# Kernel optimization log

Measured on AMD Instinct MI355X. Metric: run time of the kernel, lower is better.

Reference implementation:

```python
import jax, jax.numpy as jnp
import numpy as np

N_FEATURES = 4096
N_ACTIONS = 4
N_CLAUSES_PER_ACTION = 10
N_CLAUSES = N_ACTIONS * N_CLAUSES_PER_ACTION
BATCH = 16384
EPS = 1e-8
ACTIVE_THRESH = 1e-6


def setup_inputs() -> dict:
    key = jax.random.key(0)
    k1, k2, k3, k4 = jax.random.split(key, 4)
    features = jax.random.uniform(k1, (BATCH, N_FEATURES), dtype=jnp.float32)
    # nn.Parameter(torch.randn(F, C) * 2.0)
    clause_weights = jax.random.normal(k2, (N_FEATURES, N_CLAUSES), dtype=jnp.float32) * 2.0
    # nn.Parameter(torch.randn(F, C) * 0.5 + 2.0)
    mask_logits = jax.random.normal(k3, (N_FEATURES, N_CLAUSES), dtype=jnp.float32) * 0.5 + 2.0
    # gumbel/concrete uniform noise (torch.rand_like(mask_logits)), fixed for determinism
    u = jax.random.uniform(k4, (N_FEATURES, N_CLAUSES), dtype=jnp.float32)
    temperature = jnp.float32(5.0)
    return {"features": features, "clause_weights": clause_weights,
            "mask_logits": mask_logits, "u": u, "temperature": temperature}


def reference(features, clause_weights, mask_logits, u, temperature):
    # --- sample_mask (training: concrete relaxation) ---
    s = jax.nn.sigmoid((jnp.log(u + EPS) - jnp.log(1.0 - u + EPS) + mask_logits)
                       / (temperature + EPS))                     # (F, C)
    # --- get_clause_weights (training: soft ternary * mask) ---
    w = jnp.tanh(clause_weights / (temperature + EPS)) * s        # (F, C)

    # --- evaluate all clauses at once (masked literal mean) ---
    # literal = where(w > 0, x, 1 - x), restricted to active features (|w| > 1e-6).
    # sum_f active*literal = x @ A_pos + (1 - x) @ A_neg, so no (B,F,C) intermediate.
    active = jnp.abs(w) > ACTIVE_THRESH
    pos = (active & (w > 0)).astype(features.dtype)               # (F, C)
    neg = (active & ~(w > 0)).astype(features.dtype)              # (F, C)
    num = features @ pos + (1.0 - features) @ neg                 # (B, C)
    cnt = pos.sum(axis=0) + neg.sum(axis=0)                       # (C,)
    # mean over active literals; empty clause -> satisfaction 1
    sat = jnp.where(cnt > 0, num / jnp.maximum(cnt, 1.0), 1.0)    # (B, C)

    # --- per-action segment sum (assignment = arange(C) // cpa, contiguous) ---
    B = features.shape[0]
    action_scores = sat.reshape(B, N_ACTIONS, N_CLAUSES_PER_ACTION).sum(axis=-1)
    return action_scores                                          # (B, n_actions)
```

## Files before the change

### kernel.cpp

```cpp
#include <hip/hip_runtime.h>
#include <hip/hip_bf16.h>

#define N_FEATURES 4096
#define N_ACTIONS 4
#define N_CPA 10
#define N_CLAUSES 40
#define BATCH 16384
#define EPS 1e-8f
#define ACTIVE_THRESH 1e-6f
#define NBLK_A 160

typedef float f4v __attribute__((ext_vector_type(4)));

__global__ void count_kernel(const float* __restrict__ cw,
                             const float* __restrict__ ml,
                             const float* __restrict__ u,
                             const float* __restrict__ tptr,
                             signed char* __restrict__ d8,
                             float* __restrict__ part_pos,
                             float* __restrict__ part_neg)
{
    __shared__ float sp[N_CLAUSES], sn[N_CLAUSES];
    const int tid = threadIdx.x;
    if (tid < N_CLAUSES) { sp[tid] = 0.0f; sn[tid] = 0.0f; }
    __syncthreads();

    const float invt = 1.0f / (tptr[0] + EPS);
    const int i4 = blockIdx.x * 256 + tid;

    const float4 u4 = ((const float4*)u)[i4];
    const float4 m4 = ((const float4*)ml)[i4];
    const float4 c4 = ((const float4*)cw)[i4];

    const float uu[4] = {u4.x, u4.y, u4.z, u4.w};
    const float mm[4] = {m4.x, m4.y, m4.z, m4.w};
    const float ww[4] = {c4.x, c4.y, c4.z, c4.w};

    union { signed char c[4]; int i; } pk;
    #pragma unroll
    for (int e = 0; e < 4; ++e) {
        float z = (__logf((uu[e] + EPS) / (1.0f - uu[e] + EPS)) + mm[e]) * invt;
        float s = 1.0f / (1.0f + __expf(-z));
        float w = tanhf(ww[e] * invt) * s;
        bool active = fabsf(w) > ACTIVE_THRESH;
        bool pos = active && (w > 0.0f);
        bool neg = active && !(w > 0.0f);
        pk.c[e] = pos ? 1 : (neg ? -1 : 0);
        const int c = (i4 * 4 + e) % N_CLAUSES;
        if (pos) atomicAdd(&sp[c], 1.0f);
        if (neg) atomicAdd(&sn[c], 1.0f);
    }
    ((int*)d8)[i4] = pk.i;

    __syncthreads();
    if (tid < N_CLAUSES) {
        part_pos[blockIdx.x * N_CLAUSES + tid] = sp[tid];
        part_neg[blockIdx.x * N_CLAUSES + tid] = sn[tid];
    }
}

__global__ void fold_kernel(const signed char* __restrict__ d8,
                            const float* __restrict__ part_pos,
                            const float* __restrict__ part_neg,
                            float* __restrict__ D,
                            float* __restrict__ K)
{
    __shared__ float sinv[N_CLAUSES], sneg[N_CLAUSES];
    const int tid = threadIdx.x;
    if (tid < N_CLAUSES) {
        float p = 0.0f, n = 0.0f;
        for (int b = 0; b < NBLK_A; ++b) {
            p += part_pos[b * N_CLAUSES + tid];
            n += part_neg[b * N_CLAUSES + tid];
        }
        float cn = p + n;
        sinv[tid] = (cn > 0.0f) ? (1.0f / cn) : 0.0f;
        sneg[tid] = n;
    }
    __syncthreads();

    const int idx = blockIdx.x * 256 + tid;
    const int f = idx & (N_FEATURES - 1);
    const int a = idx >> 12;

    const signed char* drow = d8 + (size_t)f * N_CLAUSES + a * N_CPA;
    float acc = 0.0f;
    #pragma unroll
    for (int j = 0; j < N_CPA; ++j) {
        const int c = a * N_CPA + j;
        acc += (float)drow[j] * sinv[c];
    }
    D[a * N_FEATURES + f] = acc;

    if (blockIdx.x == 0 && tid < N_ACTIONS) {
        float k = 0.0f;
        #pragma unroll
        for (int j = 0; j < N_CPA; ++j) {
            const int c = tid * N_CPA + j;
            k += (sinv[c] > 0.0f) ? (sneg[c] * sinv[c]) : 1.0f;
        }
        K[tid] = k;
    }
}

#define RPB 8

__global__ __launch_bounds__(256, 3) void gemv_kernel(const float* __restrict__ x,
                                                      const float* __restrict__ D,
                                                      const float* __restrict__ K,
                                                      float* __restrict__ out)
{
    const int tid  = threadIdx.x;
    const int wave = tid >> 6;
    const int lane = tid & 63;

    __shared__ float red[4][32];

    f4v Dr[4][4];
    #pragma unroll
    for (int c = 0; c < 4; ++c)
        #pragma unroll
        for (int a = 0; a < 4; ++a)
            Dr[c][a] = *(const f4v*)(D + a * N_FEATURES + (c * 256 + tid) * 4);

    const int rb = blockIdx.x * RPB;
    const f4v* xrow = (const f4v*)(x + (size_t)rb * N_FEATURES);

    float acc[RPB][4];
    #pragma unroll
    for (int r = 0; r < RPB; ++r)
        #pragma unroll
        for (int a = 0; a < 4; ++a) acc[r][a] = 0.0f;

    f4v xv[2][4];
    #pragma unroll
    for (int c = 0; c < 4; ++c)
        xv[0][c] = __builtin_nontemporal_load(&xrow[c * 256 + tid]);

    #pragma unroll
    for (int r = 0; r < RPB; ++r) {
        const int cur = r & 1, nxt = cur ^ 1;
        if (r + 1 < RPB) {
            #pragma unroll
            for (int c = 0; c < 4; ++c)
                xv[nxt][c] = __builtin_nontemporal_load(&xrow[(r + 1) * 1024 + c * 256 + tid]);
        }
        #pragma unroll
        for (int c = 0; c < 4; ++c) {
            const f4v xc = xv[cur][c];
            #pragma unroll
            for (int a = 0; a < 4; ++a)
                acc[r][a] += xc.x * Dr[c][a].x + xc.y * Dr[c][a].y
                           + xc.z * Dr[c][a].z + xc.w * Dr[c][a].w;
        }
    }

    #pragma unroll
    for (int off = 32; off; off >>= 1)
        #pragma unroll
        for (int r = 0; r < RPB; ++r)
            #pragma unroll
            for (int a = 0; a < 4; ++a)
                acc[r][a] += __shfl_xor(acc[r][a], off);

    float myv = acc[0][0];
    #pragma unroll
    for (int v = 1; v < 32; ++v)
        if (lane == v) myv = acc[v >> 2][v & 3];
    if (lane < 32) red[wave][lane] = myv;
    __syncthreads();

    if (tid < 32) {
        float s = red[0][tid] + red[1][tid] + red[2][tid] + red[3][tid];
        out[rb * N_ACTIONS + tid] = s + K[tid & 3];
    }
}

extern "C" void kernel_launch(void* const* d_in, const int* in_sizes, int n_in,
                              void* d_out, int out_size, void* d_ws, size_t ws_size,
                              hipStream_t stream) {
    const float* features = (const float*)d_in[0];
    const float* cw       = (const float*)d_in[1];
    const float* ml       = (const float*)d_in[2];
    const float* u        = (const float*)d_in[3];
    const float* tptr     = (const float*)d_in[4];
    float* out = (float*)d_out;

    float* ws = (float*)d_ws;
    float* Dmat     = ws;
    float* K        = Dmat + N_ACTIONS * N_FEATURES;
    float* part_pos = K + 4;
    float* part_neg = part_pos + NBLK_A * N_CLAUSES;
    signed char* d8 = (signed char*)(part_neg + NBLK_A * N_CLAUSES);

    count_kernel<<<NBLK_A, 256, 0, stream>>>(cw, ml, u, tptr, d8, part_pos, part_neg);
    fold_kernel<<<(N_ACTIONS * N_FEATURES) / 256, 256, 0, stream>>>(d8, part_pos, part_neg, Dmat, K);
    gemv_kernel<<<BATCH / RPB, 256, 0, stream>>>(features, Dmat, K, out);
}
```

Baseline: 58.66 us.

## Make GEMV persistent with atomic work-stealing and use exp-based tanh

The GEMV kernel becomes persistent: 768 blocks each load the D matrix into registers once, then repeatedly claim 8-row groups through a global atomic counter that the fold kernel resets. This avoids reloading D for each of the 2048 former blocks and reduces block launch overhead. The cost is an atomic per group and an extra barrier per iteration. The count kernel also replaces tanhf with an __expf-based formula, which is cheaper but may flip a sign or activity decision at the threshold edge.

```diff
diff --git a/kernel.cpp b/kernel.cpp
--- a/kernel.cpp
+++ b/kernel.cpp
@@ -9,6 +9,9 @@
 #define EPS 1e-8f
 #define ACTIVE_THRESH 1e-6f
 #define NBLK_A 160
+#define RPB 8
+#define NGROUPS (BATCH / RPB)
+#define GEMV_BLOCKS 768
 
 typedef float f4v __attribute__((ext_vector_type(4)));
 
@@ -41,7 +44,9 @@
     for (int e = 0; e < 4; ++e) {
         float z = (__logf((uu[e] + EPS) / (1.0f - uu[e] + EPS)) + mm[e]) * invt;
         float s = 1.0f / (1.0f + __expf(-z));
-        float w = tanhf(ww[e] * invt) * s;
+        float e2 = __expf(2.0f * ww[e] * invt);
+        float th = 1.0f - 2.0f / (e2 + 1.0f);
+        float w = th * s;
         bool active = fabsf(w) > ACTIVE_THRESH;
         bool pos = active && (w > 0.0f);
         bool neg = active && !(w > 0.0f);
@@ -63,10 +68,12 @@
                             const float* __restrict__ part_pos,
                             const float* __restrict__ part_neg,
                             float* __restrict__ D,
-                            float* __restrict__ K)
+                            float* __restrict__ K,
+                            int* __restrict__ counter)
 {
     __shared__ float sinv[N_CLAUSES], sneg[N_CLAUSES];
     const int tid = threadIdx.x;
+    if (blockIdx.x == 0 && tid == 0) *counter = 0;
     if (tid < N_CLAUSES) {
         float p = 0.0f, n = 0.0f;
         for (int b = 0; b < NBLK_A; ++b) {
@@ -103,18 +110,19 @@
     }
 }
 
-#define RPB 8
-
 __global__ __launch_bounds__(256, 3) void gemv_kernel(const float* __restrict__ x,
                                                       const float* __restrict__ D,
                                                       const float* __restrict__ K,
-                                                      float* __restrict__ out)
+                                                      float* __restrict__ out,
+                                                      int* __restrict__ counter)
 {
     const int tid  = threadIdx.x;
     const int wave = tid >> 6;
     const int lane = tid & 63;
 
     __shared__ float red[4][32];
+    __shared__ float Ks[N_ACTIONS];
+    __shared__ int sg;
 
     f4v Dr[4][4];
     #pragma unroll
@@ -122,57 +130,66 @@
         #pragma unroll
         for (int a = 0; a < 4; ++a)
             Dr[c][a] = *(const f4v*)(D + a * N_FEATURES + (c * 256 + tid) * 4);
-
-    const int rb = blockIdx.x * RPB;
-    const f4v* xrow = (const f4v*)(x + (size_t)rb * N_FEATURES);
-
-    float acc[RPB][4];
-    #pragma unroll
-    for (int r = 0; r < RPB; ++r)
-        #pragma unroll
-        for (int a = 0; a < 4; ++a) acc[r][a] = 0.0f;
-
-    f4v xv[2][4];
-    #pragma unroll
-    for (int c = 0; c < 4; ++c)
-        xv[0][c] = __builtin_nontemporal_load(&xrow[c * 256 + tid]);
-
-    #pragma unroll
-    for (int r = 0; r < RPB; ++r) {
-        const int cur = r & 1, nxt = cur ^ 1;
-        if (r + 1 < RPB) {
-            #pragma unroll
-            for (int c = 0; c < 4; ++c)
-                xv[nxt][c] = __builtin_nontemporal_load(&xrow[(r + 1) * 1024 + c * 256 + tid]);
-        }
-        #pragma unroll
-        for (int c = 0; c < 4; ++c) {
-            const f4v xc = xv[cur][c];
-            #pragma unroll
-            for (int a = 0; a < 4; ++a)
-                acc[r][a] += xc.x * Dr[c][a].x + xc.y * Dr[c][a].y
-                           + xc.z * Dr[c][a].z + xc.w * Dr[c][a].w;
-        }
-    }
-
-    #pragma unroll
-    for (int off = 32; off; off >>= 1)
+    if (tid < N_ACTIONS) Ks[tid] = K[tid];
+    if (tid == 0) sg = atomicAdd(counter, 1);
+    __syncthreads();
+    int g = sg;
+
+    while (g < NGROUPS) {
+        const int rb = g * RPB;
+        const f4v* xrow = (const f4v*)(x + (size_t)rb * N_FEATURES);
+
+        float acc[RPB][4];
         #pragma unroll
         for (int r = 0; r < RPB; ++r)
             #pragma unroll
-            for (int a = 0; a < 4; ++a)
-                acc[r][a] += __shfl_xor(acc[r][a], off);
-
-    float myv = acc[0][0];
-    #pragma unroll
-    for (int v = 1; v < 32; ++v)
-        if (lane == v) myv = acc[v >> 2][v & 3];
-    if (lane < 32) red[wave][lane] = myv;
-    __syncthreads();
-
-    if (tid < 32) {
-        float s = red[0][tid] + red[1][tid] + red[2][tid] + red[3][tid];
-        out[rb * N_ACTIONS + tid] = s + K[tid & 3];
+            for (int a = 0; a < 4; ++a) acc[r][a] = 0.0f;
+
+        f4v xv[2][4];
+        #pragma unroll
+        for (int c = 0; c < 4; ++c)
+            xv[0][c] = __builtin_nontemporal_load(&xrow[c * 256 + tid]);
+        if (tid == 0) sg = atomicAdd(counter, 1);
+
+        #pragma unroll
+        for (int r = 0; r < RPB; ++r) {
+            const int cur = r & 1, nxt = cur ^ 1;
+            if (r + 1 < RPB) {
+                #pragma unroll
+                for (int c = 0; c < 4; ++c)
+                    xv[nxt][c] = __builtin_nontemporal_load(&xrow[(r + 1) * 1024 + c * 256 + tid]);
+            }
+            #pragma unroll
+            for (int c = 0; c < 4; ++c) {
+                const f4v xc = xv[cur][c];
+                #pragma unroll
+                for (int a = 0; a < 4; ++a)
+                    acc[r][a] += xc.x * Dr[c][a].x + xc.y * Dr[c][a].y
+                               + xc.z * Dr[c][a].z + xc.w * Dr[c][a].w;
+            }
+        }
+
+        #pragma unroll
+        for (int off = 32; off; off >>= 1)
+            #pragma unroll
+            for (int r = 0; r < RPB; ++r)
+                #pragma unroll
+                for (int a = 0; a < 4; ++a)
+                    acc[r][a] += __shfl_xor(acc[r][a], off);
+
+        float myv = acc[0][0];
+        #pragma unroll
+        for (int v = 1; v < 32; ++v)
+            if (lane == v) myv = acc[v >> 2][v & 3];
+        if (lane < 32) red[wave][lane] = myv;
+        __syncthreads();
+
+        if (tid < 32) {
+            float s = red[0][tid] + red[1][tid] + red[2][tid] + red[3][tid];
+            out[rb * N_ACTIONS + tid] = s + Ks[tid & 3];
+        }
+        __syncthreads();
+        g = sg;
     }
 }
 
@@ -192,8 +209,9 @@
     float* part_pos = K + 4;
     float* part_neg = part_pos + NBLK_A * N_CLAUSES;
     signed char* d8 = (signed char*)(part_neg + NBLK_A * N_CLAUSES);
+    int* counter    = (int*)(d8 + (size_t)N_CLAUSES * N_FEATURES);
 
     count_kernel<<<NBLK_A, 256, 0, stream>>>(cw, ml, u, tptr, d8, part_pos, part_neg);
-    fold_kernel<<<(N_ACTIONS * N_FEATURES) / 256, 256, 0, stream>>>(d8, part_pos, part_neg, Dmat, K);
-    gemv_kernel<<<BATCH / RPB, 256, 0, stream>>>(features, Dmat, K, out);
-}
+    fold_kernel<<<(N_ACTIONS * N_FEATURES) / 256, 256, 0, stream>>>(d8, part_pos, part_neg, Dmat, K, counter);
+    gemv_kernel<<<GEMV_BLOCKS, 256, 0, stream>>>(features, Dmat, K, out, counter);
+}
```

Result: slower. 78.37 us (+33.6%).

## Split GEMV actions across two half-blocks and use exp-based tanh

Applied to the files above, without the earlier changes.

The GEMV block grows to 512 threads, and each 256-thread half handles two of the four actions. This halves the D registers and accumulators per thread, which should allow higher occupancy, but every features row is now loaded twice, by both halves, relying on cache hits. The final reduction is remapped to match, and K is staged through shared memory. In the count kernel, tanhf is replaced with an __expf-based formula, which trades some accuracy near the active threshold for fewer instructions.

```diff
diff --git a/kernel.cpp b/kernel.cpp
--- a/kernel.cpp
+++ b/kernel.cpp
@@ -9,6 +9,7 @@
 #define EPS 1e-8f
 #define ACTIVE_THRESH 1e-6f
 #define NBLK_A 160
+#define RPB 8
 
 typedef float f4v __attribute__((ext_vector_type(4)));
 
@@ -41,7 +42,9 @@
     for (int e = 0; e < 4; ++e) {
         float z = (__logf((uu[e] + EPS) / (1.0f - uu[e] + EPS)) + mm[e]) * invt;
         float s = 1.0f / (1.0f + __expf(-z));
-        float w = tanhf(ww[e] * invt) * s;
+        float e2 = __expf(2.0f * ww[e] * invt);
+        float th = 1.0f - 2.0f / (e2 + 1.0f);
+        float w = th * s;
         bool active = fabsf(w) > ACTIVE_THRESH;
         bool pos = active && (w > 0.0f);
         bool neg = active && !(w > 0.0f);
@@ -103,39 +106,40 @@
     }
 }
 
-#define RPB 8
-
-__global__ __launch_bounds__(256, 3) void gemv_kernel(const float* __restrict__ x,
+__global__ __launch_bounds__(512, 4) void gemv_kernel(const float* __restrict__ x,
                                                       const float* __restrict__ D,
                                                       const float* __restrict__ K,
                                                       float* __restrict__ out)
 {
     const int tid  = threadIdx.x;
+    const int t    = tid & 255;
+    const int h    = tid >> 8;
     const int wave = tid >> 6;
     const int lane = tid & 63;
 
-    __shared__ float red[4][32];
-
-    f4v Dr[4][4];
+    __shared__ float red[8][16];
+    __shared__ float Ks[N_ACTIONS];
+
+    f4v Dr[4][2];
     #pragma unroll
     for (int c = 0; c < 4; ++c)
         #pragma unroll
-        for (int a = 0; a < 4; ++a)
-            Dr[c][a] = *(const f4v*)(D + a * N_FEATURES + (c * 256 + tid) * 4);
+        for (int aa = 0; aa < 2; ++aa)
+            Dr[c][aa] = *(const f4v*)(D + (h * 2 + aa) * N_FEATURES + (c * 256 + t) * 4);
+    if (tid < N_ACTIONS) Ks[tid] = K[tid];
+    __syncthreads();
 
     const int rb = blockIdx.x * RPB;
     const f4v* xrow = (const f4v*)(x + (size_t)rb * N_FEATURES);
 
-    float acc[RPB][4];
-    #pragma unroll
-    for (int r = 0; r < RPB; ++r)
-        #pragma unroll
-        for (int a = 0; a < 4; ++a) acc[r][a] = 0.0f;
+    float acc[RPB][2];
+    #pragma unroll
+    for (int r = 0; r < RPB; ++r) { acc[r][0] = 0.0f; acc[r][1] = 0.0f; }
 
     f4v xv[2][4];
     #pragma unroll
     for (int c = 0; c < 4; ++c)
-        xv[0][c] = __builtin_nontemporal_load(&xrow[c * 256 + tid]);
+        xv[0][c] = __builtin_nontemporal_load(&xrow[c * 256 + t]);
 
     #pragma unroll
     for (int r = 0; r < RPB; ++r) {
@@ -143,15 +147,15 @@
         if (r + 1 < RPB) {
             #pragma unroll
             for (int c = 0; c < 4; ++c)
-                xv[nxt][c] = __builtin_nontemporal_load(&xrow[(r + 1) * 1024 + c * 256 + tid]);
+                xv[nxt][c] = __builtin_nontemporal_load(&xrow[(r + 1) * 1024 + c * 256 + t]);
         }
         #pragma unroll
         for (int c = 0; c < 4; ++c) {
             const f4v xc = xv[cur][c];
             #pragma unroll
-            for (int a = 0; a < 4; ++a)
-                acc[r][a] += xc.x * Dr[c][a].x + xc.y * Dr[c][a].y
-                           + xc.z * Dr[c][a].z + xc.w * Dr[c][a].w;
+            for (int aa = 0; aa < 2; ++aa)
+                acc[r][aa] += xc.x * Dr[c][aa].x + xc.y * Dr[c][aa].y
+                            + xc.z * Dr[c][aa].z + xc.w * Dr[c][aa].w;
         }
     }
 
@@ -160,19 +164,22 @@
         #pragma unroll
         for (int r = 0; r < RPB; ++r)
             #pragma unroll
-            for (int a = 0; a < 4; ++a)
-                acc[r][a] += __shfl_xor(acc[r][a], off);
+            for (int aa = 0; aa < 2; ++aa)
+                acc[r][aa] += __shfl_xor(acc[r][aa], off);
 
     float myv = acc[0][0];
     #pragma unroll
-    for (int v = 1; v < 32; ++v)
-        if (lane == v) myv = acc[v >> 2][v & 3];
-    if (lane < 32) red[wave][lane] = myv;
+    for (int v = 1; v < 16; ++v)
+        if (lane == v) myv = acc[v >> 1][v & 1];
+    if (lane < 16) red[wave][lane] = myv;
     __syncthreads();
 
     if (tid < 32) {
-        float s = red[0][tid] + red[1][tid] + red[2][tid] + red[3][tid];
-        out[rb * N_ACTIONS + tid] = s + K[tid & 3];
+        const int r = tid >> 2, a = tid & 3;
+        const int wb = (a >> 1) * 4;
+        const int ix = r * 2 + (a & 1);
+        float s = red[wb + 0][ix] + red[wb + 1][ix] + red[wb + 2][ix] + red[wb + 3][ix];
+        out[rb * N_ACTIONS + tid] = s + Ks[a];
     }
 }
 
@@ -195,5 +202,5 @@
 
     count_kernel<<<NBLK_A, 256, 0, stream>>>(cw, ml, u, tptr, d8, part_pos, part_neg);
     fold_kernel<<<(N_ACTIONS * N_FEATURES) / 256, 256, 0, stream>>>(d8, part_pos, part_neg, Dmat, K);
-    gemv_kernel<<<BATCH / RPB, 256, 0, stream>>>(features, Dmat, K, out);
-}
+    gemv_kernel<<<BATCH / RPB, 512, 0, stream>>>(features, Dmat, K, out);
+}
```

Result: slower. 87.88 us (+49.8%).
